# Kernel tuning notes

Hardware: AMD Instinct MI355X
Metric: run time of the kernel (lower is better)

## Reference

```python
import jax, jax.numpy as jnp
import numpy as np

TAPS, DIMS, SPS = 32, 2, 2
LR_W, LR_F, LR_S, LR_B = 1.0 / 2**6, 1.0 / 2**7, 0.0, 1.0 / 2**11
GRAD_MAX_W, GRAD_MAX_F = 30.0, 30.0
EPS, BETA = 1e-8, 0.0


def _const16qam():
    # commplax comm.const('16QAM', norm=True): unit-average-power 16QAM grid
    p = np.array([-3.0, -1.0, 1.0, 3.0], dtype=np.float32)
    c = (p[:, None] + 1j * p[None, :]).reshape(-1) / np.sqrt(10.0)
    return jnp.asarray(c, dtype=jnp.complex64)


def _frame(x, flen, fstep):
    # xop.frame: [L, D] -> [(L-flen)//fstep + 1, flen, D]
    n = (x.shape[0] - flen) // fstep + 1
    idx = jnp.arange(n)[:, None] * fstep + jnp.arange(flen)[None, :]
    return x[idx]


def _clip(g, gmax):
    # same math as jnp.where(|g|>gmax, g/|g|*gmax, g), but NaN-safe under AD
    ag = jnp.abs(g)
    return g * jnp.minimum(1.0, gmax / jnp.maximum(ag, 1e-30))


def _ddlms(x):
    const = _const16qam()
    u_all = _frame(x, TAPS, SPS)  # [N, taps, dims] complex64

    def step(state, u):
        w, f, s, b, fshat = state
        v = jnp.einsum('ijt,tj->i', w, u)          # mimo filter output [dims]
        k = v * f
        c = k * s
        z = c + b
        q = v * fshat + b
        # decision-directed symbol (train=False, no truth)
        d = const[jnp.argmin(jnp.abs(const[:, None] - q[None, :]), axis=0)]
        psi_hat = jnp.abs(f) / f * jnp.abs(s) / s
        e_w = (d - b) * psi_hat - v
        e_f = d - b - k
        e_s = d - b - c
        e_b = d - z
        gw = -1.0 / ((jnp.abs(u) ** 2).sum() + EPS) * e_w[:, None, None] * u.conj().T[None, ...]
        gf = -1.0 / (jnp.abs(v) ** 2 + EPS) * e_f * v.conj()
        gs = -1.0 / (jnp.abs(k) ** 2 + EPS) * e_s * k.conj()
        gb = -e_b
        gw = _clip(gw, GRAD_MAX_W)
        gf = _clip(gf, GRAD_MAX_F)
        out = (w, f, s, b)  # pre-update params are used by apply
        wn = w - LR_W * gw
        fn = f - LR_F * gf
        sn = s - LR_S * gs
        bn = b - LR_B * gb
        fshatn = BETA * fshat + (1.0 - BETA) * (fn * sn)
        return (wn, fn, sn, bn, fshatn), out

    dt = jnp.complex64
    state0 = (jnp.zeros((DIMS, DIMS, TAPS), dt),   # w0 (mimoinit='zeros')
              jnp.ones((DIMS,), dt),               # f0
              jnp.ones((DIMS,), dt),               # s0
              jnp.zeros((DIMS,), dt),              # b0
              jnp.ones((DIMS,), dt))               # fshat0
    _, (ws, fs, ss, bs) = jax.lax.scan(step, state0, u_all)
    # mimo_apply: vmap(mimo)(ws, u_all) * fs * ss + bs
    y = jnp.einsum('nijt,ntj->ni', ws, u_all) * fs * ss + bs  # [N, dims]
    return y


def setup_inputs() -> dict:
    key = jax.random.key(0)
    k1, k2 = jax.random.split(key)
    x_re = jax.random.normal(k1, (200000, 2), dtype=jnp.float32)
    x_im = jax.random.normal(k2, (200000, 2), dtype=jnp.float32)
    return {"x_re": x_re, "x_im": x_im}


def reference(x_re, x_im):
    x = jax.lax.complex(x_re, x_im)  # [2N, 2] complex64
    y = _ddlms(x)                    # [(2N-taps)//sps + 1, 2] complex64
    return jnp.stack([y.real, y.imag], axis=-1)  # [N_out, 2, 2] float32
```

## Files before the change

### kernel.cpp

```cpp
#include <hip/hip_runtime.h>

typedef unsigned u2v __attribute__((ext_vector_type(2)));

#define NSTEPS 99985

template<int CTRL>
__device__ __forceinline__ float dpp_xadd(float v) {
    int s = __builtin_amdgcn_update_dpp(0, __float_as_int(v), CTRL, 0xF, 0xF, true);
    return v + __int_as_float(s);
}
#if __has_builtin(__builtin_amdgcn_permlane16_swap)
__device__ __forceinline__ float xor16_add(float v) {
    u2v r = __builtin_amdgcn_permlane16_swap((unsigned)__float_as_int(v),
                                             (unsigned)__float_as_int(v),
                                             false, false);
    return __int_as_float((int)r.x) + __int_as_float((int)r.y);
}
#else
__device__ __forceinline__ float xor16_add(float v) {
    int s = __builtin_amdgcn_ds_swizzle(__float_as_int(v), 0x401F);
    return v + __int_as_float(s);
}
#endif
__device__ __forceinline__ float red32(float v) {
    v = dpp_xadd<0xB1>(v); v = dpp_xadd<0x4E>(v);
    v = dpp_xadd<0x141>(v); v = dpp_xadd<0x140>(v);
    return xor16_add(v);
}

__device__ __forceinline__ void wave_barrier() {
    asm volatile("s_waitcnt lgkmcnt(0)" ::: "memory");
    __builtin_amdgcn_s_barrier();
    asm volatile("" ::: "memory");
}

__global__ void pre_tab(const float* __restrict__ xre,
                        const float* __restrict__ xim,
                        float4* __restrict__ tab, int ns) {
    int n = blockIdx.x * blockDim.x + threadIdx.x;
    if (n >= ns) return;
    const float* ar = xre + 4 * n;
    const float* ai = xim + 4 * n;
    float un = 0.f;
    #pragma unroll 8
    for (int k = 0; k < 64; ++k) un = fmaf(ar[k], ar[k], fmaf(ai[k], ai[k], un));
    float s = (1.0f / 64.0f) / (un + 1e-8f);
    float cr = 0.f, ci = 0.f;
    if (n + 1 < ns) {
        const float* br_ = ar + 4;
        const float* bi_ = ai + 4;
        #pragma unroll 8
        for (int k = 0; k < 64; ++k) {
            cr = fmaf(ar[k], br_[k], fmaf(ai[k], bi_[k], cr));
            ci = fmaf(ar[k], bi_[k], ci);
            ci = fmaf(-ai[k], br_[k], ci);
        }
    }
    tab[n] = make_float4(s, s * cr, s * ci, 0.f);
}

__global__ __launch_bounds__(128, 1)
void ddlms_scan2(const float* __restrict__ xre,
                 const float* __restrict__ xim,
                 const float4* __restrict__ tab,
                 float* __restrict__ out) {
    const int tid = (int)threadIdx.x;
    const int wid = tid >> 6;
    const int l = tid & 63;
    const int m = l & 31;
    const int half = l >> 5;

    constexpr float EPSv = 1e-8f;
    constexpr float LRF  = 1.0f / 128.0f;
    constexpr float LRB  = 1.0f / 2048.0f;
    const float B1 = 0.6324555320336759f;
    const float A1 = 0.31622776601683794f;
    const float A3 = 0.9486832980505138f;

    __shared__ float2 sh[8];
    if (tid < 8) sh[tid] = make_float2(0.f, 0.f);
    __syncthreads();

    float2* __restrict__ o2 = reinterpret_cast<float2*>(out);

    if (wid == 0) {
        float fr = 1.f, fi = 0.f, br = 0.f, bi = 0.f, psr = 1.f, psj = 0.f;
        float ewPr = 0.f, ewPi = 0.f, sCPr = 0.f, sCPi = 0.f;
        float4 t0 = tab[0], t1 = tab[1], t2 = tab[2], t3;

        auto W0 = [&](int n, int P, float4& tC, float4& tF) {
            wave_barrier();
            float2 bas = sh[2 * P + half];
            float Dr = fmaf(ewPr, sCPr, -(ewPi * sCPi));
            float Di = fmaf(ewPr, sCPi,   ewPi * sCPr);
            float vr = bas.x + Dr, vi = bas.y + Di;
            { int nn = n + 3; if (nn > NSTEPS - 1) nn = NSTEPS - 1; tF = tab[nn]; }

            float kr = fmaf(vr, fr, -(vi * fi));
            float ki = fmaf(vr, fi,   vi * fr);
            float zr = kr + br, zi = ki + bi;
            if (m == 0) o2[2 * n + half] = make_float2(zr, zi);

            float magr = (fabsf(zr) > B1) ? A3 : A1;
            float dr   = (zr <= 0.f) ? -magr : magr;
            float magi = (fabsf(zi) > B1) ? A3 : A1;
            float di   = (zi <= 0.f) ? -magi : magi;

            float er = dr - zr, ei = di - zi;

            float v2  = fmaf(vr, vr, fmaf(vi, vi, EPSv));
            float rv  = __builtin_amdgcn_rcpf(v2);
            float gfr = fmaf(er, vr,   ei * vi)  * rv;
            float gfi = fmaf(ei, vr, -(er * vi)) * rv;
            float m2  = fmaf(gfr, gfr, gfi * gfi);
            float scf = fminf(1.f, 30.f * __builtin_amdgcn_rsqf(m2));
            float tf  = LRF * scf;

            float dbr = dr - br, dbi = di - bi;
            float ewr = fmaf(dbr, psr, -(dbi * psj)) - vr;
            float ewi = fmaf(dbr, psj,   dbi * psr)  - vi;

            float ewsr = tC.x * ewr, ewsi = tC.x * ewi;
            if (m == 0) sh[4 + 2 * P + half] = make_float2(ewsr, ewsi);

            fr = fmaf(tf, gfr, fr); fi = fmaf(tf, gfi, fi);
            br = fmaf(LRB, er, br); bi = fmaf(LRB, ei, bi);

            float ff = fmaf(fr, fr, fi * fi);
            float rs = __builtin_amdgcn_rsqf(ff);
            psr = fr * rs; psj = -(fi * rs);

            ewPr = ewr; ewPi = ewi; sCPr = tC.y; sCPi = tC.z;
        };

        int n = 0;
        for (int it = 0; it < 24996; ++it) {
            W0(n + 0, 0, t0, t3);
            W0(n + 1, 1, t1, t0);
            W0(n + 2, 0, t2, t1);
            W0(n + 3, 1, t3, t2);
            n += 4;
        }
        W0(99984, 0, t0, t3);
    } else {
        float wAr = 0.f, wAi = 0.f, wBr = 0.f, wBi = 0.f;

        auto LOADU = [&](int nn, float& a, float& b_, float& c, float& d_) {
            const float* pr = xre + 4 * nn;
            const float* pi = xim + 4 * nn;
            a = pr[m]; c = pr[m + 32]; b_ = pi[m]; d_ = pi[m + 32];
        };

        float u0Ar, u0Ai, u0Br, u0Bi, u1Ar, u1Ai, u1Br, u1Bi,
              u2Ar, u2Ai, u2Br, u2Bi, u3Ar, u3Ai, u3Br, u3Bi;
        u3Ar = u3Ai = u3Br = u3Bi = 0.f;
        LOADU(0, u0Ar, u0Ai, u0Br, u0Bi);
        LOADU(1, u1Ar, u1Ai, u1Br, u1Bi);
        LOADU(2, u2Ar, u2Ai, u2Br, u2Bi);

        auto W1 = [&](int n, int P,
            float& uPAr, float& uPAi, float& uPBr, float& uPBi,
            float& uNAr, float& uNAi, float& uNBr, float& uNBi) {
            wave_barrier();
            float2 ews = sh[4 + 2 * (1 - P) + half];
            wAr = fmaf(ews.x, uPAr, fmaf( ews.y, uPAi, wAr));
            wAi = fmaf(ews.y, uPAr, fmaf(-ews.x, uPAi, wAi));
            wBr = fmaf(ews.x, uPBr, fmaf( ews.y, uPBi, wBr));
            wBi = fmaf(ews.y, uPBr, fmaf(-ews.x, uPBi, wBi));
            { int nn = n + 3; if (nn > NSTEPS - 1) nn = NSTEPS - 1;
              LOADU(nn, uPAr, uPAi, uPBr, uPBi); }
            float prr = wAr * uNAr; prr = fmaf(-wAi, uNAi, prr);
            prr = fmaf(wBr, uNBr, prr); prr = fmaf(-wBi, uNBi, prr);
            float pri = wAr * uNAi; pri = fmaf( wAi, uNAr, pri);
            pri = fmaf(wBr, uNBi, pri); pri = fmaf( wBi, uNBr, pri);
            float basr = red32(prr), basi = red32(pri);
            if (m == 0) sh[2 * (1 - P) + half] = make_float2(basr, basi);
        };

        int n = 0;
        for (int it = 0; it < 24996; ++it) {
            W1(n + 0, 0, u3Ar,u3Ai,u3Br,u3Bi, u1Ar,u1Ai,u1Br,u1Bi);
            W1(n + 1, 1, u0Ar,u0Ai,u0Br,u0Bi, u2Ar,u2Ai,u2Br,u2Bi);
            W1(n + 2, 0, u1Ar,u1Ai,u1Br,u1Bi, u3Ar,u3Ai,u3Br,u3Bi);
            W1(n + 3, 1, u2Ar,u2Ai,u2Br,u2Bi, u0Ar,u0Ai,u0Br,u0Bi);
            n += 4;
        }
        W1(99984, 0, u3Ar,u3Ai,u3Br,u3Bi, u1Ar,u1Ai,u1Br,u1Bi);
    }
}

__global__ __launch_bounds__(64, 1)
void ddlms_scan_fb(const float* __restrict__ xre,
                   const float* __restrict__ xim,
                   float* __restrict__ out) {
    const int l = (int)threadIdx.x;
    const int m = l & 31;
    const int half = l >> 5;
    constexpr float EPSv = 1e-8f;
    constexpr float LRW  = 1.0f / 64.0f;
    constexpr float LRF  = 1.0f / 128.0f;
    constexpr float LRB  = 1.0f / 2048.0f;
    const float B1 = 0.6324555320336759f;
    const float A1 = 0.31622776601683794f;
    const float A3 = 0.9486832980505138f;
    float wAr=0.f, wAi=0.f, wBr=0.f, wBi=0.f;
    float fr=1.f, fi=0.f, br=0.f, bi=0.f, psr=1.f, psj=0.f;
    float vr=0.f, vi=0.f, ewPr=0.f, ewPi=0.f, sP=0.f;
    float2* __restrict__ o2 = reinterpret_cast<float2*>(out);
    auto LOADU = [&](int nn, float& a, float& b_, float& c, float& d_) {
        const float* pr = xre + 4 * nn;
        const float* pi = xim + 4 * nn;
        a = pr[m]; c = pr[m + 32]; b_ = pi[m]; d_ = pi[m + 32];
    };
    float pAr,pAi,pBr,pBi, qAr,qAi,qBr,qBi, rAr,rAi,rBr,rBi;
    pAr=pAi=pBr=pBi=0.f;
    LOADU(0, qAr,qAi,qBr,qBi);
    LOADU(1, rAr,rAi,rBr,rBi);
    auto STEP = [&](int n,
        float& uPAr, float& uPAi, float& uPBr, float& uPBi,
        float& uCAr, float& uCAi, float& uCBr, float& uCBi,
        float& uNAr, float& uNAi, float& uNBr, float& uNBi) {
        {
            float gr = ewPr * uPAr; gr = fmaf( ewPi, uPAi, gr);
            float gi = ewPi * uPAr; gi = fmaf(-ewPr, uPAi, gi);
            wAr = fmaf(sP, gr, wAr); wAi = fmaf(sP, gi, wAi);
            float hr = ewPr * uPBr; hr = fmaf( ewPi, uPBi, hr);
            float hi = ewPi * uPBr; hi = fmaf(-ewPr, uPBi, hi);
            wBr = fmaf(sP, hr, wBr); wBi = fmaf(sP, hi, wBi);
        }
        float basr, basi;
        {
            float prr = wAr * uNAr; prr = fmaf(-wAi, uNAi, prr);
            prr = fmaf(wBr, uNBr, prr); prr = fmaf(-wBi, uNBi, prr);
            float pri = wAr * uNAi; pri = fmaf( wAi, uNAr, pri);
            pri = fmaf(wBr, uNBi, pri); pri = fmaf( wBi, uNBr, pri);
            basr = red32(prr); basi = red32(pri);
        }
        float uu = uCAr*uCAr; uu = fmaf(uCAi,uCAi,uu);
        uu = fmaf(uCBr,uCBr,uu); uu = fmaf(uCBi,uCBi,uu);
        float sN = LRW * __builtin_amdgcn_rcpf(red32(uu) + EPSv);
        float ccr = uCAr*uNAr; ccr = fmaf(uCAi,uNAi,ccr);
        ccr = fmaf(uCBr,uNBr,ccr); ccr = fmaf(uCBi,uNBi,ccr);
        float cci = uCAr*uNAi; cci = fmaf(-uCAi,uNAr,cci);
        cci = fmaf(uCBr,uNBi,cci); cci = fmaf(-uCBi,uNBr,cci);
        float sCr = sN * red32(ccr), sCi = sN * red32(cci);
        float kr = fmaf(vr, fr, -(vi * fi));
        float ki = fmaf(vr, fi,   vi * fr);
        float zr = kr + br, zi = ki + bi;
        if (m == 0) o2[2 * n + half] = make_float2(zr, zi);
        float magr = (fabsf(zr) > B1) ? A3 : A1;
        float dr   = (zr <= 0.f) ? -magr : magr;
        float magi = (fabsf(zi) > B1) ? A3 : A1;
        float di   = (zi <= 0.f) ? -magi : magi;
        float er = dr - zr, ei = di - zi;
        float v2  = fmaf(vr, vr, fmaf(vi, vi, EPSv));
        float rv  = __builtin_amdgcn_rcpf(v2);
        float gfr = fmaf(er, vr,   ei * vi)  * rv;
        float gfi = fmaf(ei, vr, -(er * vi)) * rv;
        float m2  = fmaf(gfr, gfr, gfi * gfi);
        float scf = fminf(1.f, 30.f * __builtin_amdgcn_rsqf(m2));
        float tf  = LRF * scf;
        float dbr = dr - br, dbi = di - bi;
        float ewr = fmaf(dbr, psr, -(dbi * psj)) - vr;
        float ewi = fmaf(dbr, psj,   dbi * psr)  - vi;
        float Dr = fmaf(ewr, sCr, -(ewi * sCi));
        float Di = fmaf(ewr, sCi,   ewi * sCr);
        vr = basr + Dr; vi = basi + Di;
        fr = fmaf(tf, gfr, fr); fi = fmaf(tf, gfi, fi);
        br = fmaf(LRB, er, br); bi = fmaf(LRB, ei, bi);
        float ff = fmaf(fr, fr, fi * fi);
        float rs = __builtin_amdgcn_rsqf(ff);
        psr = fr * rs; psj = -(fi * rs);
        ewPr = ewr; ewPi = ewi; sP = sN;
        int nn = n + 2; if (nn > NSTEPS - 1) nn = NSTEPS - 1;
        LOADU(nn, uPAr, uPAi, uPBr, uPBi);
    };
    int n = 0;
    for (int it = 0; it < 33328; ++it) {
        STEP(n,     pAr,pAi,pBr,pBi,  qAr,qAi,qBr,qBi,  rAr,rAi,rBr,rBi);
        STEP(n + 1, qAr,qAi,qBr,qBi,  rAr,rAi,rBr,rBi,  pAr,pAi,pBr,pBi);
        STEP(n + 2, rAr,rAi,rBr,rBi,  pAr,pAi,pBr,pBi,  qAr,qAi,qBr,qBi);
        n += 3;
    }
    STEP(99984, pAr,pAi,pBr,pBi, qAr,qAi,qBr,qBi, rAr,rAi,rBr,rBi);
}

extern "C" void kernel_launch(void* const* d_in, const int* in_sizes, int n_in,
                              void* d_out, int out_size, void* d_ws, size_t ws_size,
                              hipStream_t stream) {
    const float* xre = (const float*)d_in[0];
    const float* xim = (const float*)d_in[1];
    float* out = (float*)d_out;

    if (ws_size >= (size_t)NSTEPS * sizeof(float4)) {
        float4* tab = (float4*)d_ws;
        pre_tab<<<(NSTEPS + 255) / 256, 256, 0, stream>>>(xre, xim, tab, NSTEPS);
        ddlms_scan2<<<1, 128, 0, stream>>>(xre, xim, tab, out);
    } else {
        ddlms_scan_fb<<<1, 64, 0, stream>>>(xre, xim, out);
    }
}
```

Baseline: 19.84 ms.

## Deepen wave pipeline using lag-1..3 cross-correlation table to shorten critical path

The precompute kernel now stores, per step, the cross-correlations of the current frame with the previous three frames, packed into two float4 entries. This lets the filter wave compute its base output one step further ahead, with the recent error contributions patched in from the table. The control wave's critical path per step shrinks, with a 4-slot shared ring instead of 2. The custom wave barrier is replaced by __syncthreads, and the table doubles in size with three times the precompute work.

New measurement: 29.81 ms. +50.2%, slower.

```diff
diff --git a/kernel.cpp b/kernel.cpp
--- a/kernel.cpp
+++ b/kernel.cpp
@@ -2,7 +2,7 @@
 
 typedef unsigned u2v __attribute__((ext_vector_type(2)));
 
-#define NSTEPS 99985
+#define NS 99985
 
 template<int CTRL>
 __device__ __forceinline__ float dpp_xadd(float v) {
@@ -28,15 +28,9 @@
     return xor16_add(v);
 }
 
-__device__ __forceinline__ void wave_barrier() {
-    asm volatile("s_waitcnt lgkmcnt(0)" ::: "memory");
-    __builtin_amdgcn_s_barrier();
-    asm volatile("" ::: "memory");
-}
-
-__global__ void pre_tab(const float* __restrict__ xre,
-                        const float* __restrict__ xim,
-                        float4* __restrict__ tab, int ns) {
+__global__ void pre_tab8(const float* __restrict__ xre,
+                         const float* __restrict__ xim,
+                         float4* __restrict__ tab8, int ns) {
     int n = blockIdx.x * blockDim.x + threadIdx.x;
     if (n >= ns) return;
     const float* ar = xre + 4 * n;
@@ -45,24 +39,30 @@
     #pragma unroll 8
     for (int k = 0; k < 64; ++k) un = fmaf(ar[k], ar[k], fmaf(ai[k], ai[k], un));
     float s = (1.0f / 64.0f) / (un + 1e-8f);
-    float cr = 0.f, ci = 0.f;
-    if (n + 1 < ns) {
-        const float* br_ = ar + 4;
-        const float* bi_ = ai + 4;
-        #pragma unroll 8
-        for (int k = 0; k < 64; ++k) {
-            cr = fmaf(ar[k], br_[k], fmaf(ai[k], bi_[k], cr));
-            ci = fmaf(ar[k], bi_[k], ci);
-            ci = fmaf(-ai[k], br_[k], ci);
+    float C[3][2] = {{0,0},{0,0},{0,0}};
+    #pragma unroll
+    for (int j = 1; j <= 3; ++j) {
+        if (n >= j) {
+            const float* pr = ar - 4 * j;
+            const float* pi = ai - 4 * j;
+            float cr = 0.f, ci = 0.f;
+            #pragma unroll 8
+            for (int k = 0; k < 64; ++k) {
+                cr = fmaf(pr[k], ar[k], fmaf(pi[k], ai[k], cr));
+                ci = fmaf(pr[k], ai[k], ci);
+                ci = fmaf(-pi[k], ar[k], ci);
+            }
+            C[j - 1][0] = cr; C[j - 1][1] = ci;
         }
     }
-    tab[n] = make_float4(s, s * cr, s * ci, 0.f);
+    tab8[2 * n]     = make_float4(s, C[0][0], C[0][1], C[2][0]);
+    tab8[2 * n + 1] = make_float4(C[2][1], C[1][0], C[1][1], 0.f);
 }
 
 __global__ __launch_bounds__(128, 1)
 void ddlms_scan2(const float* __restrict__ xre,
                  const float* __restrict__ xim,
-                 const float4* __restrict__ tab,
+                 const float4* __restrict__ tab8,
                  float* __restrict__ out) {
     const int tid = (int)threadIdx.x;
     const int wid = tid >> 6;
@@ -77,24 +77,40 @@
     const float A1 = 0.31622776601683794f;
     const float A3 = 0.9486832980505138f;
 
-    __shared__ float2 sh[8];
-    if (tid < 8) sh[tid] = make_float2(0.f, 0.f);
+    __shared__ float2 sh[16];
+    if (tid < 16) sh[tid] = make_float2(0.f, 0.f);
     __syncthreads();
 
     float2* __restrict__ o2 = reinterpret_cast<float2*>(out);
 
     if (wid == 0) {
         float fr = 1.f, fi = 0.f, br = 0.f, bi = 0.f, psr = 1.f, psj = 0.f;
-        float ewPr = 0.f, ewPi = 0.f, sCPr = 0.f, sCPi = 0.f;
-        float4 t0 = tab[0], t1 = tab[1], t2 = tab[2], t3;
-
-        auto W0 = [&](int n, int P, float4& tC, float4& tF) {
-            wave_barrier();
-            float2 bas = sh[2 * P + half];
-            float Dr = fmaf(ewPr, sCPr, -(ewPi * sCPi));
-            float Di = fmaf(ewPr, sCPi,   ewPi * sCPr);
-            float vr = bas.x + Dr, vi = bas.y + Di;
-            { int nn = n + 3; if (nn > NSTEPS - 1) nn = NSTEPS - 1; tF = tab[nn]; }
+        float e1r = 0.f, e1i = 0.f;
+        float partR = 0.f, partI = 0.f;
+
+        float t0s=0,t0c1r=0,t0c1i=0,t0c2r=0,t0c2i=0;
+        float t1s=0,t1c1r=0,t1c1i=0,t1c2r=0,t1c2i=0;
+        float t2s=0,t2c1r=0,t2c1i=0,t2c2r=0,t2c2i=0;
+        float t3s=0,t3c1r=0,t3c1i=0,t3c2r=0,t3c2i=0;
+        auto LOADT = [&](int nn, float& s, float& c1r, float& c1i,
+                         float& c2r, float& c2i) {
+            if (nn > NS - 1) nn = NS - 1;
+            float4 a = tab8[2 * nn], b = tab8[2 * nn + 1];
+            s = a.x; c1r = a.y; c1i = a.z; c2r = b.y; c2i = b.z;
+        };
+        LOADT(0, t0s,t0c1r,t0c1i,t0c2r,t0c2i);
+        LOADT(1, t1s,t1c1r,t1c1i,t1c2r,t1c2i);
+        LOADT(2, t2s,t2c1r,t2c1i,t2c2r,t2c2i);
+
+        auto W0 = [&](int n, float tCs, float tCc1r, float tCc1i,
+                      float tNc2r, float tNc2i,
+                      float& tFs, float& tFc1r, float& tFc1i,
+                      float& tFc2r, float& tFc2i) {
+            __syncthreads();
+            float2 pN = sh[((n + 1) & 3) * 2 + half];
+
+            float vr = fmaf(e1r, tCc1r, partR); vr = fmaf(-e1i, tCc1i, vr);
+            float vi = fmaf(e1r, tCc1i, partI); vi = fmaf( e1i, tCc1r, vi);
 
             float kr = fmaf(vr, fr, -(vi * fi));
             float ki = fmaf(vr, fi,   vi * fr);
@@ -120,8 +136,8 @@
             float ewr = fmaf(dbr, psr, -(dbi * psj)) - vr;
             float ewi = fmaf(dbr, psj,   dbi * psr)  - vi;
 
-            float ewsr = tC.x * ewr, ewsi = tC.x * ewi;
-            if (m == 0) sh[4 + 2 * P + half] = make_float2(ewsr, ewsi);
+            float ewsr = tCs * ewr, ewsi = tCs * ewi;
+            if (m == 0) sh[8 + (n & 3) * 2 + half] = make_float2(ewsr, ewsi);
 
             fr = fmaf(tf, gfr, fr); fi = fmaf(tf, gfi, fi);
             br = fmaf(LRB, er, br); bi = fmaf(LRB, ei, bi);
@@ -130,62 +146,86 @@
             float rs = __builtin_amdgcn_rsqf(ff);
             psr = fr * rs; psj = -(fi * rs);
 
-            ewPr = ewr; ewPi = ewi; sCPr = tC.y; sCPi = tC.z;
+            partR = fmaf(e1r, tNc2r, pN.x); partR = fmaf(-e1i, tNc2i, partR);
+            partI = fmaf(e1r, tNc2i, pN.y); partI = fmaf( e1i, tNc2r, partI);
+
+            e1r = ewsr; e1i = ewsi;
+
+            LOADT(n + 3, tFs, tFc1r, tFc1i, tFc2r, tFc2i);
         };
 
         int n = 0;
         for (int it = 0; it < 24996; ++it) {
-            W0(n + 0, 0, t0, t3);
-            W0(n + 1, 1, t1, t0);
-            W0(n + 2, 0, t2, t1);
-            W0(n + 3, 1, t3, t2);
+            W0(n+0, t0s,t0c1r,t0c1i, t1c2r,t1c2i, t3s,t3c1r,t3c1i,t3c2r,t3c2i);
+            W0(n+1, t1s,t1c1r,t1c1i, t2c2r,t2c2i, t0s,t0c1r,t0c1i,t0c2r,t0c2i);
+            W0(n+2, t2s,t2c1r,t2c1i, t3c2r,t3c2i, t1s,t1c1r,t1c1i,t1c2r,t1c2i);
+            W0(n+3, t3s,t3c1r,t3c1i, t0c2r,t0c2i, t2s,t2c1r,t2c1i,t2c2r,t2c2i);
             n += 4;
         }
-        W0(99984, 0, t0, t3);
+        W0(99984, t0s,t0c1r,t0c1i, t1c2r,t1c2i,
+                  t3s,t3c1r,t3c1i,t3c2r,t3c2i);
     } else {
         float wAr = 0.f, wAi = 0.f, wBr = 0.f, wBi = 0.f;
 
         auto LOADU = [&](int nn, float& a, float& b_, float& c, float& d_) {
+            if (nn > NS - 1) nn = NS - 1;
             const float* pr = xre + 4 * nn;
             const float* pi = xim + 4 * nn;
             a = pr[m]; c = pr[m + 32]; b_ = pi[m]; d_ = pi[m + 32];
         };
-
-        float u0Ar, u0Ai, u0Br, u0Bi, u1Ar, u1Ai, u1Br, u1Bi,
-              u2Ar, u2Ai, u2Br, u2Bi, u3Ar, u3Ai, u3Br, u3Bi;
+        float c3r0=0,c3i0=0, c3r1=0,c3i1=0, c3r2=0,c3i2=0, c3r3=0,c3i3=0;
+        auto LOADT3 = [&](int nn, float& c3r, float& c3i) {
+            if (nn > NS - 1) nn = NS - 1;
+            float4 a = tab8[2 * nn], b = tab8[2 * nn + 1];
+            c3r = a.w; c3i = b.x;
+        };
+        LOADT3(2, c3r2, c3i2); LOADT3(3, c3r3, c3i3);
+        LOADT3(4, c3r0, c3i0); LOADT3(5, c3r1, c3i1);
+
+        float u0Ar,u0Ai,u0Br,u0Bi, u1Ar,u1Ai,u1Br,u1Bi,
+              u2Ar,u2Ai,u2Br,u2Bi, u3Ar,u3Ai,u3Br,u3Bi;
         u3Ar = u3Ai = u3Br = u3Bi = 0.f;
         LOADU(0, u0Ar, u0Ai, u0Br, u0Bi);
         LOADU(1, u1Ar, u1Ai, u1Br, u1Bi);
         LOADU(2, u2Ar, u2Ai, u2Br, u2Bi);
 
-        auto W1 = [&](int n, int P,
+        auto W1 = [&](int k,
             float& uPAr, float& uPAi, float& uPBr, float& uPBi,
-            float& uNAr, float& uNAi, float& uNBr, float& uNBi) {
-            wave_barrier();
-            float2 ews = sh[4 + 2 * (1 - P) + half];
+            float uQAr, float uQAi, float uQBr, float uQBi,
+            float tQc3r, float tQc3i,
+            float& tFc3r, float& tFc3i) {
+            __syncthreads();
+            float2 ews = sh[8 + ((k - 1) & 3) * 2 + half];
+            float prr = wAr * uQAr; prr = fmaf(-wAi, uQAi, prr);
+            prr = fmaf(wBr, uQBr, prr); prr = fmaf(-wBi, uQBi, prr);
+            float pri = wAr * uQAi; pri = fmaf( wAi, uQAr, pri);
+            pri = fmaf(wBr, uQBi, pri); pri = fmaf( wBi, uQBr, pri);
+            float pre2r = red32(prr), pre2i = red32(pri);
             wAr = fmaf(ews.x, uPAr, fmaf( ews.y, uPAi, wAr));
             wAi = fmaf(ews.y, uPAr, fmaf(-ews.x, uPAi, wAi));
             wBr = fmaf(ews.x, uPBr, fmaf( ews.y, uPBi, wBr));
             wBi = fmaf(ews.y, uPBr, fmaf(-ews.x, uPBi, wBi));
-            { int nn = n + 3; if (nn > NSTEPS - 1) nn = NSTEPS - 1;
-              LOADU(nn, uPAr, uPAi, uPBr, uPBi); }
-            float prr = wAr * uNAr; prr = fmaf(-wAi, uNAi, prr);
-            prr = fmaf(wBr, uNBr, prr); prr = fmaf(-wBi, uNBi, prr);
-            float pri = wAr * uNAi; pri = fmaf( wAi, uNAr, pri);
-            pri = fmaf(wBr, uNBi, pri); pri = fmaf( wBi, uNBr, pri);
-            float basr = red32(prr), basi = red32(pri);
-            if (m == 0) sh[2 * (1 - P) + half] = make_float2(basr, basi);
-        };
-
-        int n = 0;
+            float PRr = fmaf(ews.x, tQc3r, fmaf(-ews.y, tQc3i, pre2r));
+            float PRi = fmaf(ews.x, tQc3i, fmaf( ews.y, tQc3r, pre2i));
+            if (m == 0) sh[((k + 2) & 3) * 2 + half] = make_float2(PRr, PRi);
+            LOADU(k + 3, uPAr, uPAi, uPBr, uPBi);
+            LOADT3(k + 6, tFc3r, tFc3i);
+        };
+
+        int k = 0;
         for (int it = 0; it < 24996; ++it) {
-            W1(n + 0, 0, u3Ar,u3Ai,u3Br,u3Bi, u1Ar,u1Ai,u1Br,u1Bi);
-            W1(n + 1, 1, u0Ar,u0Ai,u0Br,u0Bi, u2Ar,u2Ai,u2Br,u2Bi);
-            W1(n + 2, 0, u1Ar,u1Ai,u1Br,u1Bi, u3Ar,u3Ai,u3Br,u3Bi);
-            W1(n + 3, 1, u2Ar,u2Ai,u2Br,u2Bi, u0Ar,u0Ai,u0Br,u0Bi);
-            n += 4;
-        }
-        W1(99984, 0, u3Ar,u3Ai,u3Br,u3Bi, u1Ar,u1Ai,u1Br,u1Bi);
+            W1(k+0, u3Ar,u3Ai,u3Br,u3Bi, u2Ar,u2Ai,u2Br,u2Bi,
+                    c3r2,c3i2, c3r2,c3i2);
+            W1(k+1, u0Ar,u0Ai,u0Br,u0Bi, u3Ar,u3Ai,u3Br,u3Bi,
+                    c3r3,c3i3, c3r3,c3i3);
+            W1(k+2, u1Ar,u1Ai,u1Br,u1Bi, u0Ar,u0Ai,u0Br,u0Bi,
+                    c3r0,c3i0, c3r0,c3i0);
+            W1(k+3, u2Ar,u2Ai,u2Br,u2Bi, u1Ar,u1Ai,u1Br,u1Bi,
+                    c3r1,c3i1, c3r1,c3i1);
+            k += 4;
+        }
+        W1(99984, u3Ar,u3Ai,u3Br,u3Bi, u2Ar,u2Ai,u2Br,u2Bi,
+                  c3r2,c3i2, c3r2,c3i2);
     }
 }
 
@@ -272,7 +312,7 @@
         float rs = __builtin_amdgcn_rsqf(ff);
         psr = fr * rs; psj = -(fi * rs);
         ewPr = ewr; ewPi = ewi; sP = sN;
-        int nn = n + 2; if (nn > NSTEPS - 1) nn = NSTEPS - 1;
+        int nn = n + 2; if (nn > NS - 1) nn = NS - 1;
         LOADU(nn, uPAr, uPAi, uPBr, uPBi);
     };
     int n = 0;
@@ -292,10 +332,10 @@
     const float* xim = (const float*)d_in[1];
     float* out = (float*)d_out;
 
-    if (ws_size >= (size_t)NSTEPS * sizeof(float4)) {
-        float4* tab = (float4*)d_ws;
-        pre_tab<<<(NSTEPS + 255) / 256, 256, 0, stream>>>(xre, xim, tab, NSTEPS);
-        ddlms_scan2<<<1, 128, 0, stream>>>(xre, xim, tab, out);
+    if (ws_size >= (size_t)2 * NS * sizeof(float4)) {
+        float4* tab8 = (float4*)d_ws;
+        pre_tab8<<<(NS + 255) / 256, 256, 0, stream>>>(xre, xim, tab8, NS);
+        ddlms_scan2<<<1, 128, 0, stream>>>(xre, xim, tab8, out);
     } else {
         ddlms_scan_fb<<<1, 64, 0, stream>>>(xre, xim, out);
     }
```
